# Kernel tuning notes

Measured on AMD Instinct MI355X. Metric: run time of the kernel, lower is better.

Reference implementation:

```python
import jax, jax.numpy as jnp
import numpy as np

EPS = 1e-6
GROUPS = 32  # min(C//4, 32) with C=256

def group_norm(x, scale, bias):
    B, H, W, C = x.shape
    g = GROUPS
    xg = x.reshape(B, H, W, g, C // g)
    mean = jnp.mean(xg, axis=(1, 2, 4), keepdims=True)
    var = jnp.var(xg, axis=(1, 2, 4), keepdims=True)
    xg = (xg - mean) * jax.lax.rsqrt(var + EPS)
    return xg.reshape(B, H, W, C) * scale + bias

def nin(x, w, b):
    return jnp.einsum('bhwc,cd->bhwd', x, w) + b

def setup_inputs() -> dict:
    key = jax.random.key(0)
    ks = jax.random.split(key, 11)
    B, H, W, C = 8, 64, 64, 256
    s = 1.0 / np.sqrt(C)
    return {
        'x': jax.random.normal(ks[0], (B, H, W, C), jnp.float32),
        'gn_scale': jnp.ones((C,), jnp.float32),
        'gn_bias': jnp.zeros((C,), jnp.float32),
        'Wq': jax.random.normal(ks[1], (C, C), jnp.float32) * s,
        'bq': jnp.zeros((C,), jnp.float32),
        'Wk': jax.random.normal(ks[2], (C, C), jnp.float32) * s,
        'bk': jnp.zeros((C,), jnp.float32),
        'Wv': jax.random.normal(ks[3], (C, C), jnp.float32) * s,
        'bv': jnp.zeros((C,), jnp.float32),
        'Wo': jax.random.normal(ks[4], (C, C), jnp.float32) * s * 0.1,
        'bo': jnp.zeros((C,), jnp.float32),
    }

def reference(x, gn_scale, gn_bias, Wq, bq, Wk, bk, Wv, bv, Wo, bo):
    B, H, W, C = x.shape
    h = group_norm(x, gn_scale, gn_bias)
    q = nin(h, Wq, bq)
    k = nin(h, Wk, bk)
    v = nin(h, Wv, bv)
    w = jnp.einsum('bhwc,bHWc->bhwHW', q, k) * (C ** -0.5)
    w = w.reshape(B, H, W, H * W)
    w = jax.nn.softmax(w, axis=-1)
    w = w.reshape(B, H, W, H, W)
    h = jnp.einsum('bhwHW,bHWc->bhwc', w, v)
    h = nin(h, Wo, bo)
    return x + h
```

## Files before the change

kernel.cpp:

```cpp
#include <hip/hip_runtime.h>
#include <stdint.h>

using short8 = __attribute__((ext_vector_type(8))) short;
using f32x4  = __attribute__((ext_vector_type(4))) float;

#define L2E 1.44269504088896f

static __device__ __forceinline__ unsigned short f2bf(float f) {
  union { float f; uint32_t u; } v; v.f = f;
  uint32_t r = v.u + 0x7fffu + ((v.u >> 16) & 1u);
  return (unsigned short)(r >> 16);
}
static __device__ __forceinline__ float bf2f(unsigned short u) {
  union { uint32_t u; float f; } v; v.u = ((uint32_t)u) << 16;
  return v.f;
}

static __device__ __forceinline__ void gload16(const unsigned short* g, unsigned short* l) {
  __builtin_amdgcn_global_load_lds(
      (const __attribute__((address_space(1))) void*)g,
      (__attribute__((address_space(3))) void*)l, 16, 0, 0);
}

static __device__ __forceinline__ float red_add_lg(float x) {
  x += __shfl_xor(x, 16);
  x += __shfl_xor(x, 32);
  return x;
}
static __device__ __forceinline__ float red_max_lg(float x) {
  x = fmaxf(x, __shfl_xor(x, 16));
  x = fmaxf(x, __shfl_xor(x, 32));
  return x;
}

__global__ __launch_bounds__(256) void prep_w(
    const float* __restrict__ Wq, const float* __restrict__ Wk,
    const float* __restrict__ Wv, const float* __restrict__ Wo,
    unsigned short* __restrict__ Wt) {
  int k = threadIdx.x, d = blockIdx.x, w = blockIdx.y;
  const float* src = (w==0)?Wq:(w==1)?Wk:(w==2)?Wv:Wo;
  Wt[w*65536 + d*256 + k] = f2bf(src[k*256 + d]);
}

__global__ __launch_bounds__(256) void gn_stats(
    const float* __restrict__ x, float* __restrict__ part) {
  int c = threadIdx.x, ch = blockIdx.x, b = blockIdx.y;
  float s = 0.f, q = 0.f;
  const float* p = x + ((b*4096) + ch*64)*256 + c;
  for (int it = 0; it < 64; ++it) {
    float v = p[it*256];
    s += v; q += v*v;
  }
  s += __shfl_xor(s,1); q += __shfl_xor(q,1);
  s += __shfl_xor(s,2); q += __shfl_xor(q,2);
  s += __shfl_xor(s,4); q += __shfl_xor(q,4);
  if ((c & 7) == 0) {
    int g = c >> 3;
    part[((b*64 + ch)*32 + g)*2 + 0] = s;
    part[((b*64 + ch)*32 + g)*2 + 1] = q;
  }
}

__global__ __launch_bounds__(256) void gn_apply(
    const float* __restrict__ x, const float* __restrict__ part,
    const float* __restrict__ sc, const float* __restrict__ bi,
    unsigned short* __restrict__ h) {
  int c = threadIdx.x, ch = blockIdx.x, b = blockIdx.y;
  int g = c >> 3;
  float s = 0.f, q = 0.f;
  for (int cc = 0; cc < 64; ++cc) {
    s += part[((b*64 + cc)*32 + g)*2 + 0];
    q += part[((b*64 + cc)*32 + g)*2 + 1];
  }
  float mean = s * (1.f/32768.f);
  float var  = q * (1.f/32768.f) - mean*mean;
  float rstd = rsqrtf(var + 1e-6f);
  float a  = rstd * sc[c];
  float d0 = bi[c] - mean * a;
  const float* p = x + ((b*4096) + ch*64)*256 + c;
  unsigned short* o = h + ((b*4096) + ch*64)*256 + c;
  for (int it = 0; it < 64; ++it)
    o[it*256] = f2bf(p[it*256] * a + d0);
}

__global__ __launch_bounds__(256) void gemm_qkvt(
    const unsigned short* __restrict__ A,
    const unsigned short* __restrict__ Wt,
    const float* __restrict__ bq,
    const float* __restrict__ bk,
    const float* __restrict__ bv,
    unsigned short* __restrict__ Qout,
    unsigned short* __restrict__ Kout,
    unsigned short* __restrict__ Vt) {
  int bid = blockIdx.x;
  int tid = threadIdx.x;
  int w = tid >> 6, l = tid & 63, lr = l & 15, lg = l >> 4;
  if (bid < 512) {
    const unsigned short* Wtq = Wt;
    const unsigned short* Wtk = Wt + 65536;
    int i0 = bid * 64;
    int j0 = w * 64;
    f32x4 accq[4][4] = {}, acck[4][4] = {};
#pragma unroll
    for (int kk = 0; kk < 8; ++kk) {
      short8 af[4], bfq[4], bfk[4];
#pragma unroll
      for (int mi = 0; mi < 4; ++mi)
        af[mi] = *(const short8*)(A + (i0 + mi*16 + lr)*256 + kk*32 + lg*8);
#pragma unroll
      for (int ni = 0; ni < 4; ++ni) {
        bfq[ni] = *(const short8*)(Wtq + (j0 + ni*16 + lr)*256 + kk*32 + lg*8);
        bfk[ni] = *(const short8*)(Wtk + (j0 + ni*16 + lr)*256 + kk*32 + lg*8);
      }
#pragma unroll
      for (int mi = 0; mi < 4; ++mi)
#pragma unroll
        for (int ni = 0; ni < 4; ++ni) {
          accq[mi][ni] = __builtin_amdgcn_mfma_f32_16x16x32_bf16(af[mi], bfq[ni], accq[mi][ni], 0,0,0);
          acck[mi][ni] = __builtin_amdgcn_mfma_f32_16x16x32_bf16(af[mi], bfk[ni], acck[mi][ni], 0,0,0);
        }
    }
#pragma unroll
    for (int mi = 0; mi < 4; ++mi) {
#pragma unroll
      for (int ni = 0; ni < 4; ++ni) {
        int j = j0 + ni*16 + lr;
#pragma unroll
        for (int r = 0; r < 4; ++r) {
          int i = i0 + mi*16 + lg*4 + r;
          Qout[i*256 + j] = f2bf((accq[mi][ni][r] + bq[j]) * 0.0625f);
          Kout[i*256 + j] = f2bf(acck[mi][ni][r] + bk[j]);
        }
      }
    }
  } else {
    const unsigned short* Wtv = Wt + 131072;
    int v = bid - 512;
    int i0 = (v & 3) * 64;
    int j0 = (v >> 2) * 256 + w * 64;
    f32x4 acc[4][4] = {};
#pragma unroll
    for (int kk = 0; kk < 8; ++kk) {
      short8 af[4], bfr[4];
#pragma unroll
      for (int mi = 0; mi < 4; ++mi)
        af[mi] = *(const short8*)(Wtv + (i0 + mi*16 + lr)*256 + kk*32 + lg*8);
#pragma unroll
      for (int ni = 0; ni < 4; ++ni)
        bfr[ni] = *(const short8*)(A + (j0 + ni*16 + lr)*256 + kk*32 + lg*8);
#pragma unroll
      for (int mi = 0; mi < 4; ++mi)
#pragma unroll
        for (int ni = 0; ni < 4; ++ni)
          acc[mi][ni] = __builtin_amdgcn_mfma_f32_16x16x32_bf16(af[mi], bfr[ni], acc[mi][ni], 0,0,0);
    }
#pragma unroll
    for (int mi = 0; mi < 4; ++mi) {
#pragma unroll
      for (int ni = 0; ni < 4; ++ni) {
        int j = j0 + ni*16 + lr;
#pragma unroll
        for (int r = 0; r < 4; ++r) {
          int i = i0 + mi*16 + lg*4 + r;
          int idx = ((j >> 12) << 20) + i*4096 + (j & 4095);
          Vt[idx] = f2bf(acc[mi][ni][r] + bv[i]);
        }
      }
    }
  }
}

__global__ __launch_bounds__(256) void gemm_bt(
    const unsigned short* __restrict__ A,
    const unsigned short* __restrict__ Bm,
    const float* __restrict__ bias_n,
    const float* __restrict__ resid,
    float* __restrict__ outp) {
  int tid = threadIdx.x;
  int w = tid >> 6, l = tid & 63, lr = l & 15, lg = l >> 4;
  int i0 = blockIdx.x * 64;
  int j0 = w * 64;
  f32x4 acc[4][4] = {};
#pragma unroll
  for (int kk = 0; kk < 8; ++kk) {
    short8 af[4], bfr[4];
#pragma unroll
    for (int mi = 0; mi < 4; ++mi)
      af[mi] = *(const short8*)(A + (i0 + mi*16 + lr)*256 + kk*32 + lg*8);
#pragma unroll
    for (int ni = 0; ni < 4; ++ni)
      bfr[ni] = *(const short8*)(Bm + (j0 + ni*16 + lr)*256 + kk*32 + lg*8);
#pragma unroll
    for (int mi = 0; mi < 4; ++mi)
#pragma unroll
      for (int ni = 0; ni < 4; ++ni)
        acc[mi][ni] = __builtin_amdgcn_mfma_f32_16x16x32_bf16(af[mi], bfr[ni], acc[mi][ni], 0,0,0);
  }
#pragma unroll
  for (int mi = 0; mi < 4; ++mi) {
#pragma unroll
    for (int ni = 0; ni < 4; ++ni) {
      int j = j0 + ni*16 + lr;
#pragma unroll
      for (int r = 0; r < 4; ++r) {
        int i = i0 + mi*16 + lg*4 + r;
        outp[i*256 + j] = acc[mi][ni][r] + bias_n[j] + resid[i*256 + j];
      }
    }
  }
}

__global__ __launch_bounds__(256) void gemm_fin(
    const unsigned short* __restrict__ P0,
    const unsigned short* __restrict__ P1,
    const float* __restrict__ stats,
    const unsigned short* __restrict__ Bm,
    const float* __restrict__ bias_n,
    const float* __restrict__ resid,
    float* __restrict__ outp) {
  int tid = threadIdx.x;
  int w = tid >> 6, l = tid & 63, lr = l & 15, lg = l >> 4;
  int i0 = blockIdx.x * 64;
  int j0 = w * 64;
  float a1m[4], a2m[4];
#pragma unroll
  for (int mi = 0; mi < 4; ++mi) {
    int row = i0 + mi*16 + lr;
    float m1 = stats[row*2 + 0],           l1 = stats[row*2 + 1];
    float m2 = stats[65536 + row*2 + 0],   l2 = stats[65536 + row*2 + 1];
    float M  = fmaxf(m1, m2);
    float a1 = __builtin_amdgcn_exp2f((m1 - M) * L2E);
    float a2 = __builtin_amdgcn_exp2f((m2 - M) * L2E);
    float inv = 1.f / (a1*l1 + a2*l2);
    a1m[mi] = a1 * inv; a2m[mi] = a2 * inv;
  }
  f32x4 acc[4][4] = {};
#pragma unroll
  for (int kk = 0; kk < 8; ++kk) {
    short8 af[4], bfr[4];
#pragma unroll
    for (int mi = 0; mi < 4; ++mi) {
      int off = (i0 + mi*16 + lr)*256 + kk*32 + lg*8;
      short8 v1 = *(const short8*)(P0 + off);
      short8 v2 = *(const short8*)(P1 + off);
      union { unsigned int u[4]; short8 s8; } pk;
#pragma unroll
      for (int e = 0; e < 4; ++e) {
        float g0 = bf2f((unsigned short)v1[2*e])   * a1m[mi] + bf2f((unsigned short)v2[2*e])   * a2m[mi];
        float g1 = bf2f((unsigned short)v1[2*e+1]) * a1m[mi] + bf2f((unsigned short)v2[2*e+1]) * a2m[mi];
        asm("v_cvt_pk_bf16_f32 %0, %1, %2" : "=v"(pk.u[e]) : "v"(g0), "v"(g1));
      }
      af[mi] = pk.s8;
    }
#pragma unroll
    for (int ni = 0; ni < 4; ++ni)
      bfr[ni] = *(const short8*)(Bm + (j0 + ni*16 + lr)*256 + kk*32 + lg*8);
#pragma unroll
    for (int mi = 0; mi < 4; ++mi)
#pragma unroll
      for (int ni = 0; ni < 4; ++ni)
        acc[mi][ni] = __builtin_amdgcn_mfma_f32_16x16x32_bf16(af[mi], bfr[ni], acc[mi][ni], 0,0,0);
  }
#pragma unroll
  for (int mi = 0; mi < 4; ++mi) {
#pragma unroll
    for (int ni = 0; ni < 4; ++ni) {
      int j = j0 + ni*16 + lr;
#pragma unroll
      for (int r = 0; r < 4; ++r) {
        int i = i0 + mi*16 + lg*4 + r;
        outp[i*256 + j] = acc[mi][ni][r] + bias_n[j] + resid[i*256 + j];
      }
    }
  }
}

static __device__ __forceinline__ void stage_kv32(
    const unsigned short* __restrict__ Kb, const unsigned short* __restrict__ Vb,
    int kt, unsigned short* dK, unsigned short* dV, int w, int l) {
#pragma unroll
  for (int i = 0; i < 4; ++i) {
    int t = (w*4 + i)*64 + l;
    int r = t >> 5, cs = t & 31;
    int cg = cs ^ (r & 7);
    gload16(Kb + (kt*32 + r)*256 + cg*8, dK + t*8);
  }
#pragma unroll
  for (int i = 0; i < 4; ++i) {
    int t = (w*4 + i)*64 + l;
    int d = t >> 2, s = t & 3;
    int sg = s ^ ((d ^ (d >> 2)) & 3);
    gload16(Vb + d*4096 + kt*32 + sg*8, dV + t*8);
  }
}

__global__ __launch_bounds__(256, 2) void attn_fwd(
    const unsigned short* __restrict__ Q,
    const unsigned short* __restrict__ Kmat,
    const unsigned short* __restrict__ Vt,
    unsigned short* __restrict__ P0,
    unsigned short* __restrict__ P1,
    float* __restrict__ stats) {
  __shared__ __align__(16) unsigned short ldsK[2][32][256];
  __shared__ __align__(16) unsigned short ldsV[2][256][32];

  int tid = threadIdx.x;
  int w = tid >> 6, l = tid & 63, lr = l & 15, lg = l >> 4;
  int b  = blockIdx.x & 7;
  int mt = (blockIdx.x >> 3) & 31;
  int ks = blockIdx.x >> 8;
  int m0 = mt*128 + w*32;
  int sw = lr & 7;
  int vsw = (lr ^ (lr >> 2)) & 3;
  int lgp = ((lg & 1) << 1) | (lg >> 1);

  const unsigned short* Kb = Kmat + b*(4096*256) + ks*(2048*256);
  const unsigned short* Vb = Vt   + (b << 20) + ks*2048;
  unsigned short* Pp = ks ? P1 : P0;

  short8 qf[2][8];
#pragma unroll
  for (int qn = 0; qn < 2; ++qn) {
    int qbase = ((b*4096) + m0 + qn*16 + lr)*256 + lg*8;
#pragma unroll
    for (int kk = 0; kk < 8; ++kk)
      qf[qn][kk] = *(const short8*)(Q + qbase + kk*32);
  }

  float mrun[2], lrun[2];
  f32x4 oacc[2][16] = {};
  mrun[0] = mrun[1] = -1e30f;
  lrun[0] = lrun[1] = 0.f;

  stage_kv32(Kb, Vb, 0, &ldsK[0][0][0], &ldsV[0][0][0], w, l);

  for (int kt = 0; kt < 64; ++kt) {
    int cur = kt & 1;
    if (kt < 63) {
      stage_kv32(Kb, Vb, kt+1, &ldsK[cur^1][0][0], &ldsV[cur^1][0][0], w, l);
      asm volatile("s_waitcnt vmcnt(8)" ::: "memory");
    } else {
      asm volatile("s_waitcnt vmcnt(0)" ::: "memory");
    }
    __builtin_amdgcn_s_barrier();
    __builtin_amdgcn_sched_barrier(0);

    const unsigned short (*Kc)[256] = ldsK[cur];
    const unsigned short (*Vc)[32]  = ldsV[cur];

    f32x4 s_[2][2];
#pragma unroll
    for (int qn = 0; qn < 2; ++qn)
#pragma unroll
      for (int kn = 0; kn < 2; ++kn) s_[qn][kn] = (f32x4){0.f,0.f,0.f,0.f};
#pragma unroll
    for (int kn = 0; kn < 2; ++kn) {
#pragma unroll
      for (int kk = 0; kk < 8; ++kk) {
        short8 kf = *(const short8*)&Kc[kn*16 + lr][((kk*4 + lg) ^ sw)*8];
        s_[0][kn] = __builtin_amdgcn_mfma_f32_16x16x32_bf16(kf, qf[0][kk], s_[0][kn], 0,0,0);
        s_[1][kn] = __builtin_amdgcn_mfma_f32_16x16x32_bf16(kf, qf[1][kk], s_[1][kn], 0,0,0);
      }
    }

    short8 pa[2];
#pragma unroll
    for (int qn = 0; qn < 2; ++qn) {
      float ma = fmaxf(fmaxf(s_[qn][0][0], s_[qn][0][1]), fmaxf(s_[qn][0][2], s_[qn][0][3]));
      float mb = fmaxf(fmaxf(s_[qn][1][0], s_[qn][1][1]), fmaxf(s_[qn][1][2], s_[qn][1][3]));
      float pmax = fmaxf(ma, mb);
      if (__any(pmax > mrun[qn] + 8.f)) {
        float mx = red_max_lg(pmax);
        float mnew = fmaxf(mrun[qn], mx);
        float alpha = __builtin_amdgcn_exp2f((mrun[qn] - mnew) * L2E);
        mrun[qn] = mnew;
        lrun[qn] *= alpha;
        float at[4];
#pragma unroll
        for (int r = 0; r < 4; ++r) at[r] = __shfl(alpha, lg*4 + r);
#pragma unroll
        for (int jt = 0; jt < 16; ++jt)
#pragma unroll
          for (int r = 0; r < 4; ++r) oacc[qn][jt][r] *= at[r];
      }
      float mL = mrun[qn] * L2E;
      float p[2][4];
#pragma unroll
      for (int kn = 0; kn < 2; ++kn)
#pragma unroll
        for (int r = 0; r < 4; ++r)
          p[kn][r] = __builtin_amdgcn_exp2f(s_[qn][kn][r]*L2E - mL);
      float t0 = (p[0][0]+p[0][1]) + (p[0][2]+p[0][3]);
      float t1 = (p[1][0]+p[1][1]) + (p[1][2]+p[1][3]);
      lrun[qn] += red_add_lg(t0 + t1);
      unsigned int X0, X1, Y0, Y1;
      asm("v_cvt_pk_bf16_f32 %0, %1, %2" : "=v"(X0) : "v"(p[0][0]), "v"(p[0][1]));
      asm("v_cvt_pk_bf16_f32 %0, %1, %2" : "=v"(X1) : "v"(p[0][2]), "v"(p[0][3]));
      asm("v_cvt_pk_bf16_f32 %0, %1, %2" : "=v"(Y0) : "v"(p[1][0]), "v"(p[1][1]));
      asm("v_cvt_pk_bf16_f32 %0, %1, %2" : "=v"(Y1) : "v"(p[1][2]), "v"(p[1][3]));
      asm("v_permlane16_swap_b32 %0, %1" : "+v"(X0), "+v"(Y0));
      asm("v_permlane16_swap_b32 %0, %1" : "+v"(X1), "+v"(Y1));
      union { unsigned int u[4]; short8 s8; } pk;
      pk.u[0] = X0; pk.u[1] = X1; pk.u[2] = Y0; pk.u[3] = Y1;
      pa[qn] = pk.s8;
    }

#pragma unroll
    for (int jt = 0; jt < 16; ++jt) {
      short8 vf = *(const short8*)&Vc[jt*16 + lr][(lgp ^ vsw)*8];
      oacc[0][jt] = __builtin_amdgcn_mfma_f32_16x16x32_bf16(pa[0], vf, oacc[0][jt], 0,0,0);
      oacc[1][jt] = __builtin_amdgcn_mfma_f32_16x16x32_bf16(pa[1], vf, oacc[1][jt], 0,0,0);
    }
    __builtin_amdgcn_sched_barrier(0);
    __builtin_amdgcn_s_barrier();
  }

  if (lg == 0) {
#pragma unroll
    for (int qn = 0; qn < 2; ++qn) {
      int row = b*4096 + m0 + qn*16 + lr;
      stats[(ks*32768 + row)*2 + 0] = mrun[qn];
      stats[(ks*32768 + row)*2 + 1] = lrun[qn];
    }
  }
#pragma unroll
  for (int qn = 0; qn < 2; ++qn) {
#pragma unroll
    for (int r = 0; r < 4; ++r) {
      int row = ((b*4096) + m0 + qn*16 + lg*4 + r)*256;
#pragma unroll
      for (int jt = 0; jt < 16; ++jt)
        Pp[row + jt*16 + lr] = f2bf(oacc[qn][jt][r]);
    }
  }
}

__global__ __launch_bounds__(256) void merge_attn(
    const unsigned short* __restrict__ P0,
    const unsigned short* __restrict__ P1,
    const float* __restrict__ stats,
    unsigned short* __restrict__ Out) {
  int tid = threadIdx.x;
  int row = blockIdx.x*8 + (tid >> 5);
  int c8  = (tid & 31) * 8;
  float m1 = stats[row*2 + 0],          l1 = stats[row*2 + 1];
  float m2 = stats[(32768 + row)*2 + 0], l2 = stats[(32768 + row)*2 + 1];
  float M  = fmaxf(m1, m2);
  float a1 = __builtin_amdgcn_exp2f((m1 - M) * L2E);
  float a2 = __builtin_amdgcn_exp2f((m2 - M) * L2E);
  float inv = 1.f / (a1*l1 + a2*l2);
  a1 *= inv; a2 *= inv;
  short8 v1 = *(const short8*)(P0 + row*256 + c8);
  short8 v2 = *(const short8*)(P1 + row*256 + c8);
  union { unsigned short u[8]; short8 s8; } o;
#pragma unroll
  for (int j = 0; j < 8; ++j)
    o.u[j] = f2bf(bf2f((unsigned short)v1[j])*a1 + bf2f((unsigned short)v2[j])*a2);
  *(short8*)(Out + row*256 + c8) = o.s8;
}

extern "C" void kernel_launch(void* const* d_in, const int* in_sizes, int n_in,
                              void* d_out, int out_size, void* d_ws, size_t ws_size,
                              hipStream_t stream) {
  (void)in_sizes; (void)n_in; (void)out_size;
  const float* x  = (const float*)d_in[0];
  const float* gs = (const float*)d_in[1];
  const float* gb = (const float*)d_in[2];
  const float* Wq = (const float*)d_in[3];
  const float* bq = (const float*)d_in[4];
  const float* Wk = (const float*)d_in[5];
  const float* bk = (const float*)d_in[6];
  const float* Wv = (const float*)d_in[7];
  const float* bv = (const float*)d_in[8];
  const float* Wo = (const float*)d_in[9];
  const float* bo = (const float*)d_in[10];

  char* ws = (char*)d_ws;
  unsigned short* h  = (unsigned short*)(ws);
  unsigned short* Qb = (unsigned short*)(ws + (size_t)16777216);
  unsigned short* Kb = (unsigned short*)(ws + (size_t)33554432);
  unsigned short* Vt = (unsigned short*)(ws + (size_t)50331648);
  unsigned short* Wt = (unsigned short*)(ws + (size_t)67108864);
  float* part        = (float*)(ws + (size_t)67633152);
  float* stats       = (float*)(ws + (size_t)67764224);
  unsigned short* P1ws = (unsigned short*)(ws + (size_t)68288512);
  bool fuse = (ws_size >= (size_t)68288512 + 16777216);
  unsigned short* Op1 = fuse ? P1ws : (unsigned short*)d_out;

  prep_w  <<<dim3(256,4), 256, 0, stream>>>(Wq, Wk, Wv, Wo, Wt);
  gn_stats<<<dim3(64,8),  256, 0, stream>>>(x, part);
  gn_apply<<<dim3(64,8),  256, 0, stream>>>(x, part, gs, gb, h);
  gemm_qkvt<<<dim3(1024), 256, 0, stream>>>(h, Wt, bq, bk, bv, Qb, Kb, Vt);
  attn_fwd<<<dim3(512),  256, 0, stream>>>(Qb, Kb, Vt, h, Op1, stats);
  if (fuse) {
    gemm_fin<<<dim3(512), 256, 0, stream>>>(h, P1ws, stats, Wt+196608, bo, x, (float*)d_out);
  } else {
    merge_attn<<<dim3(4096), 256, 0, stream>>>(h, Op1, stats, Qb);
    gemm_bt<<<dim3(512), 256, 0, stream>>>(Qb, Wt+196608, bo, x, (float*)d_out);
  }
}
```

Measured before the change: 297.0 us.

## Fuse group-norm apply into QKV GEMM operand loads

The gn_apply kernel is replaced by a small gn_coef kernel that computes per-batch, per-channel scale and shift coefficients. The QKV/V^T GEMM now reads fp32 x directly, applies the affine normalization in registers and converts to bf16 with v_cvt_pk_bf16_f32 when building MFMA fragments. This removes a full pass that wrote the normalized bf16 activation and read it back. In exchange, the GEMM loads fp32 data, twice the bytes of bf16, and the V^T blocks reread x several times, so it depends on L2 reuse. It also does extra FMA and convert work per fragment.

```diff
diff --git a/kernel.cpp b/kernel.cpp
--- a/kernel.cpp
+++ b/kernel.cpp
@@ -31,6 +31,28 @@
   x = fmaxf(x, __shfl_xor(x, 16));
   x = fmaxf(x, __shfl_xor(x, 32));
   return x;
+}
+
+static __device__ __forceinline__ short8 gn_frag(
+    const float* __restrict__ xp, f32x4 ca0, f32x4 ca1, f32x4 cd0, f32x4 cd1) {
+  f32x4 x0 = *(const f32x4*)xp;
+  f32x4 x1 = *(const f32x4*)(xp + 4);
+  float g0 = fmaf(x0[0], ca0[0], cd0[0]);
+  float g1 = fmaf(x0[1], ca0[1], cd0[1]);
+  float g2 = fmaf(x0[2], ca0[2], cd0[2]);
+  float g3 = fmaf(x0[3], ca0[3], cd0[3]);
+  float g4 = fmaf(x1[0], ca1[0], cd1[0]);
+  float g5 = fmaf(x1[1], ca1[1], cd1[1]);
+  float g6 = fmaf(x1[2], ca1[2], cd1[2]);
+  float g7 = fmaf(x1[3], ca1[3], cd1[3]);
+  unsigned int u0, u1, u2, u3;
+  asm("v_cvt_pk_bf16_f32 %0, %1, %2" : "=v"(u0) : "v"(g0), "v"(g1));
+  asm("v_cvt_pk_bf16_f32 %0, %1, %2" : "=v"(u1) : "v"(g2), "v"(g3));
+  asm("v_cvt_pk_bf16_f32 %0, %1, %2" : "=v"(u2) : "v"(g4), "v"(g5));
+  asm("v_cvt_pk_bf16_f32 %0, %1, %2" : "=v"(u3) : "v"(g6), "v"(g7));
+  union { unsigned int u[4]; short8 s8; } pk;
+  pk.u[0] = u0; pk.u[1] = u1; pk.u[2] = u2; pk.u[3] = u3;
+  return pk.s8;
 }
 
 __global__ __launch_bounds__(256) void prep_w(
@@ -61,11 +83,11 @@
   }
 }
 
-__global__ __launch_bounds__(256) void gn_apply(
-    const float* __restrict__ x, const float* __restrict__ part,
+__global__ __launch_bounds__(256) void gn_coef(
+    const float* __restrict__ part,
     const float* __restrict__ sc, const float* __restrict__ bi,
-    unsigned short* __restrict__ h) {
-  int c = threadIdx.x, ch = blockIdx.x, b = blockIdx.y;
+    float* __restrict__ agn, float* __restrict__ dgn) {
+  int c = threadIdx.x, b = blockIdx.x;
   int g = c >> 3;
   float s = 0.f, q = 0.f;
   for (int cc = 0; cc < 64; ++cc) {
@@ -76,15 +98,13 @@
   float var  = q * (1.f/32768.f) - mean*mean;
   float rstd = rsqrtf(var + 1e-6f);
   float a  = rstd * sc[c];
-  float d0 = bi[c] - mean * a;
-  const float* p = x + ((b*4096) + ch*64)*256 + c;
-  unsigned short* o = h + ((b*4096) + ch*64)*256 + c;
-  for (int it = 0; it < 64; ++it)
-    o[it*256] = f2bf(p[it*256] * a + d0);
+  agn[b*256 + c] = a;
+  dgn[b*256 + c] = bi[c] - mean * a;
 }
 
 __global__ __launch_bounds__(256) void gemm_qkvt(
-    const unsigned short* __restrict__ A,
+    const float* __restrict__ x,
+    const float* __restrict__ agn, const float* __restrict__ dgn,
     const unsigned short* __restrict__ Wt,
     const float* __restrict__ bq,
     const float* __restrict__ bk,
@@ -92,9 +112,14 @@
     unsigned short* __restrict__ Qout,
     unsigned short* __restrict__ Kout,
     unsigned short* __restrict__ Vt) {
+  __shared__ float aco[256], dco[256];
   int bid = blockIdx.x;
   int tid = threadIdx.x;
   int w = tid >> 6, l = tid & 63, lr = l & 15, lg = l >> 4;
+  int b = (bid < 512) ? (bid >> 6) : ((bid - 512) >> 6);
+  aco[tid] = agn[b*256 + tid];
+  dco[tid] = dgn[b*256 + tid];
+  __syncthreads();
   if (bid < 512) {
     const unsigned short* Wtq = Wt;
     const unsigned short* Wtk = Wt + 65536;
@@ -103,14 +128,19 @@
     f32x4 accq[4][4] = {}, acck[4][4] = {};
 #pragma unroll
     for (int kk = 0; kk < 8; ++kk) {
+      int k0 = kk*32 + lg*8;
+      f32x4 ca0 = *(const f32x4*)&aco[k0];
+      f32x4 ca1 = *(const f32x4*)&aco[k0 + 4];
+      f32x4 cd0 = *(const f32x4*)&dco[k0];
+      f32x4 cd1 = *(const f32x4*)&dco[k0 + 4];
       short8 af[4], bfq[4], bfk[4];
 #pragma unroll
       for (int mi = 0; mi < 4; ++mi)
-        af[mi] = *(const short8*)(A + (i0 + mi*16 + lr)*256 + kk*32 + lg*8);
+        af[mi] = gn_frag(x + (i0 + mi*16 + lr)*256 + k0, ca0, ca1, cd0, cd1);
 #pragma unroll
       for (int ni = 0; ni < 4; ++ni) {
-        bfq[ni] = *(const short8*)(Wtq + (j0 + ni*16 + lr)*256 + kk*32 + lg*8);
-        bfk[ni] = *(const short8*)(Wtk + (j0 + ni*16 + lr)*256 + kk*32 + lg*8);
+        bfq[ni] = *(const short8*)(Wtq + (j0 + ni*16 + lr)*256 + k0);
+        bfk[ni] = *(const short8*)(Wtk + (j0 + ni*16 + lr)*256 + k0);
       }
 #pragma unroll
       for (int mi = 0; mi < 4; ++mi)
@@ -141,13 +171,18 @@
     f32x4 acc[4][4] = {};
 #pragma unroll
     for (int kk = 0; kk < 8; ++kk) {
+      int k0 = kk*32 + lg*8;
+      f32x4 ca0 = *(const f32x4*)&aco[k0];
+      f32x4 ca1 = *(const f32x4*)&aco[k0 + 4];
+      f32x4 cd0 = *(const f32x4*)&dco[k0];
+      f32x4 cd1 = *(const f32x4*)&dco[k0 + 4];
       short8 af[4], bfr[4];
 #pragma unroll
       for (int mi = 0; mi < 4; ++mi)
-        af[mi] = *(const short8*)(Wtv + (i0 + mi*16 + lr)*256 + kk*32 + lg*8);
+        af[mi] = *(const short8*)(Wtv + (i0 + mi*16 + lr)*256 + k0);
 #pragma unroll
       for (int ni = 0; ni < 4; ++ni)
-        bfr[ni] = *(const short8*)(A + (j0 + ni*16 + lr)*256 + kk*32 + lg*8);
+        bfr[ni] = gn_frag(x + (j0 + ni*16 + lr)*256 + k0, ca0, ca1, cd0, cd1);
 #pragma unroll
       for (int mi = 0; mi < 4; ++mi)
 #pragma unroll
@@ -484,13 +519,15 @@
   float* part        = (float*)(ws + (size_t)67633152);
   float* stats       = (float*)(ws + (size_t)67764224);
   unsigned short* P1ws = (unsigned short*)(ws + (size_t)68288512);
+  float* agn = (float*)ws;
+  float* dgn = (float*)(ws + 8192);
   bool fuse = (ws_size >= (size_t)68288512 + 16777216);
   unsigned short* Op1 = fuse ? P1ws : (unsigned short*)d_out;
 
   prep_w  <<<dim3(256,4), 256, 0, stream>>>(Wq, Wk, Wv, Wo, Wt);
   gn_stats<<<dim3(64,8),  256, 0, stream>>>(x, part);
-  gn_apply<<<dim3(64,8),  256, 0, stream>>>(x, part, gs, gb, h);
-  gemm_qkvt<<<dim3(1024), 256, 0, stream>>>(h, Wt, bq, bk, bv, Qb, Kb, Vt);
+  gn_coef <<<dim3(8),     256, 0, stream>>>(part, gs, gb, agn, dgn);
+  gemm_qkvt<<<dim3(1024), 256, 0, stream>>>(x, agn, dgn, Wt, bq, bk, bv, Qb, Kb, Vt);
   attn_fwd<<<dim3(512),  256, 0, stream>>>(Qb, Kb, Vt, h, Op1, stats);
   if (fuse) {
     gemm_fin<<<dim3(512), 256, 0, stream>>>(h, P1ws, stats, Wt+196608, bo, x, (float*)d_out);
```

Measured after the change: 302.9 us. No clear change (+2.0%).
